# Optimization experiments

Hardware: AMD Instinct MI355X
Metric: run time of the kernel (lower is better)

The kernel has to match this reference:

```python
import jax, jax.numpy as jnp
import numpy as np

B, TY, ENC, EMB, DEC, V = 16, 255, 512, 256, 512, 32000
EPS = 1e-5


def _lstm(x, Wih, Whh, bih, bhh):
    # x: [B, T, Din]; torch gate order i, f, g, o; h0 = c0 = 0
    Bb = x.shape[0]
    H = Whh.shape[1]
    xw = jnp.einsum('btd,gd->btg', x, Wih) + bih + bhh  # [B, T, 4H]

    def step(carry, xt):
        h, c = carry
        g = xt + h @ Whh.T
        i, f, gg, o = jnp.split(g, 4, axis=-1)
        i = jax.nn.sigmoid(i)
        f = jax.nn.sigmoid(f)
        gg = jnp.tanh(gg)
        o = jax.nn.sigmoid(o)
        c = f * c + i * gg
        h = o * jnp.tanh(c)
        return (h, c), h

    h0 = jnp.zeros((Bb, H), x.dtype)
    _, hs = jax.lax.scan(step, (h0, h0), jnp.swapaxes(xw, 0, 1))
    return jnp.swapaxes(hs, 0, 1)  # [B, T, H]


def setup_inputs():
    key = jax.random.key(0)
    ks = jax.random.split(key, 16)
    s = 0.05
    rn = lambda k, sh: jax.random.normal(k, sh, jnp.float32)
    return {
        'x': rn(ks[0], (B, ENC)),
        'y': jax.random.randint(ks[1], (B, TY), 0, V),
        'fc1_w': rn(ks[2], (EMB, ENC)) * s,
        'fc1_b': rn(ks[3], (EMB,)) * s,
        'bn_g': jnp.ones((EMB,), jnp.float32),
        'bn_b': jnp.zeros((EMB,), jnp.float32),
        'emb': rn(ks[4], (V, EMB)) * s,
        'l1_Wih': rn(ks[5], (4 * DEC, EMB)) * s,
        'l1_Whh': rn(ks[6], (4 * DEC, DEC)) * s,
        'l1_bih': rn(ks[7], (4 * DEC,)) * s,
        'l1_bhh': rn(ks[8], (4 * DEC,)) * s,
        'attn_Wout': rn(ks[9], (DEC, 2 * DEC)) * s,
        'dc_Wih': rn(ks[10], (4 * DEC, DEC)) * s,
        'dc_Whh': rn(ks[11], (4 * DEC, DEC)) * s,
        'dc_bih': rn(ks[12], (4 * DEC,)) * s,
        'dc_bhh': rn(ks[13], (4 * DEC,)) * s,
        'fc2_w': rn(ks[14], (V, DEC)) * s,
        'fc2_b': rn(ks[15], (V,)) * s,
        'lengths': TY + 1,  # all sequences full length
    }


def reference(x, y, fc1_w, fc1_b, bn_g, bn_b, emb, l1_Wih, l1_Whh, l1_bih, l1_bhh,
              attn_Wout, dc_Wih, dc_Whh, dc_bih, dc_bhh, fc2_w, fc2_b, lengths):
    # fc1 + BatchNorm1d (training-mode batch stats, biased var)
    feat = x @ fc1_w.T + fc1_b                         # [B, EMB]
    mu = feat.mean(axis=0)
    var = feat.var(axis=0)
    feat = (feat - mu) / jnp.sqrt(var + EPS) * bn_g + bn_b
    # prepend feature to embedded tokens -> [B, L, EMB], L = TY + 1
    seq = jnp.concatenate([feat[:, None, :], emb[y]], axis=1)
    # first LSTM
    h = _lstm(seq, l1_Wih, l1_Whh, l1_bih, l1_bhh)     # [B, L, DEC]
    L = seq.shape[1]
    # causal dot-product self-attention (vectorized form of the python loop)
    scores = jnp.einsum('bqd,bkd->bqk', h, h)
    mask = jnp.tril(jnp.ones((L, L), bool))
    w = jax.nn.softmax(jnp.where(mask, scores, -1e30), axis=-1)
    mix = jnp.einsum('bqk,bkd->bqd', w, h)
    attn = jnp.tanh(jnp.concatenate([mix, h], axis=-1) @ attn_Wout.T)
    # decoder LSTM cell over attended features
    out = _lstm(attn, dc_Wih, dc_Whh, dc_bih, dc_bhh)  # [B, L, DEC]
    return out @ fc2_w.T + fc2_b                       # [B, L, V]
```

## Files before the change

kernel.cpp:

```cpp
#include <hip/hip_runtime.h>

#define BB 16
#define TY 255
#define ENC 512
#define EMBD 256
#define DEC 512
#define VV 32000
#define LL 256
#define M4 4096
#define GG 2048
#define SENT 0x7FC0

typedef unsigned short u16;
typedef __attribute__((ext_vector_type(8))) short short8;
typedef __attribute__((ext_vector_type(4))) float f32x4;
typedef __attribute__((ext_vector_type(4))) unsigned short u16x4;

__device__ __forceinline__ u16 f2bf(float f) {
  unsigned u = __float_as_uint(f);
  u += 0x7fff + ((u >> 16) & 1);
  return (u16)(u >> 16);
}
__device__ __forceinline__ f32x4 mfma16(short8 a, short8 b, f32x4 c) {
  return __builtin_amdgcn_mfma_f32_16x16x32_bf16(a, b, c, 0, 0, 0);
}
__device__ __forceinline__ float sigmoidf_(float x) { return 1.f / (1.f + expf(-x)); }

__device__ __forceinline__ void st_b32_dev(int* a, int v) {
  asm volatile("global_store_dword %0, %1, off sc1" :: "v"(a), "v"(v) : "memory");
}
__device__ __forceinline__ void gload_lds16(const u16* g, u16* l) {
  __builtin_amdgcn_global_load_lds(
      (const __attribute__((address_space(1))) void*)g,
      (__attribute__((address_space(3))) void*)l, 16, 0, 0);
}

template<bool BT, bool OBF, bool DOTANH, bool BIAS>
__global__ __launch_bounds__(256) void gemm_kernel(
    const u16* __restrict__ A, const u16* __restrict__ Bm, void* __restrict__ Cv,
    const float* __restrict__ bias,
    int K, int lda, int ldb, int ldc,
    long a_bs, long b_bs, long c_bs)
{
  __shared__ u16 As[64][72];
  __shared__ u16 Bs[64][72];
  const int tid = threadIdx.x;
  const long m0 = (long)blockIdx.y * 64, n0 = (long)blockIdx.x * 64;
  const int z = blockIdx.z;
  const u16* Ab = A + (long)z * a_bs;
  const u16* Bb = Bm + (long)z * b_bs;
  const int lane = tid & 63, w = tid >> 6;
  const int wm = w >> 1, wn = w & 1;
  f32x4 acc[2][2] = {};
  for (int k0 = 0; k0 < K; k0 += 64) {
#pragma unroll
    for (int i = 0; i < 2; i++) {
      int c = tid + 256 * i;
      int r = c >> 3, kk = (c & 7) << 3;
      *(short8*)&As[r][kk] = *(const short8*)&Ab[(m0 + r) * (long)lda + k0 + kk];
    }
    if (BT) {
#pragma unroll
      for (int i = 0; i < 2; i++) {
        int c = tid + 256 * i;
        int r = c >> 3, kk = (c & 7) << 3;
        *(short8*)&Bs[r][kk] = *(const short8*)&Bb[(n0 + r) * (long)ldb + k0 + kk];
      }
    } else {
#pragma unroll
      for (int i = 0; i < 2; i++) {
        int c = tid + 256 * i;
        int kk = c >> 3, nn = (c & 7) << 3;
        const u16* s = &Bb[(long)(k0 + kk) * ldb + n0 + nn];
#pragma unroll
        for (int j = 0; j < 8; j++) Bs[nn + j][kk] = s[j];
      }
    }
    __syncthreads();
#pragma unroll
    for (int kf = 0; kf < 2; kf++) {
      const int ko = kf * 32 + (lane >> 4) * 8;
      short8 a0 = *(const short8*)&As[wm * 32 + (lane & 15)][ko];
      short8 a1 = *(const short8*)&As[wm * 32 + 16 + (lane & 15)][ko];
      short8 b0 = *(const short8*)&Bs[wn * 32 + (lane & 15)][ko];
      short8 b1 = *(const short8*)&Bs[wn * 32 + 16 + (lane & 15)][ko];
      acc[0][0] = mfma16(a0, b0, acc[0][0]);
      acc[0][1] = mfma16(a0, b1, acc[0][1]);
      acc[1][0] = mfma16(a1, b0, acc[1][0]);
      acc[1][1] = mfma16(a1, b1, acc[1][1]);
    }
    __syncthreads();
  }
#pragma unroll
  for (int m = 0; m < 2; m++)
#pragma unroll
    for (int n = 0; n < 2; n++) {
#pragma unroll
      for (int r = 0; r < 4; r++) {
        long row = m0 + wm * 32 + m * 16 + (lane >> 4) * 4 + r;
        long col = n0 + wn * 32 + n * 16 + (lane & 15);
        float v = acc[m][n][r];
        if (BIAS) v += bias[col];
        if (DOTANH) v = tanhf(v);
        if (OBF) ((u16*)Cv)[(long)z * c_bs + row * ldc + col] = f2bf(v);
        else ((float*)Cv)[(long)z * c_bs + row * ldc + col] = v;
      }
    }
}

template<bool OBF, bool DOTANH, bool BIAS, bool CAUSAL3>
__global__ __launch_bounds__(256) void gemm128_kernel(
    const u16* __restrict__ A, const u16* __restrict__ Bm, void* __restrict__ Cv,
    const float* __restrict__ bias,
    int K, int lda, int ldb, int ldc,
    long a_bs, long b_bs, long c_bs)
{
  __shared__ u16 As[128 * 64];
  __shared__ u16 Bs[128 * 64];
  const int tid = threadIdx.x;
  long m0, n0;
  if (CAUSAL3) {
    int id = blockIdx.x;
    m0 = (id > 0) ? 128 : 0;
    n0 = (id > 1) ? 128 : 0;
  } else {
    m0 = (long)blockIdx.y * 128;
    n0 = (long)blockIdx.x * 128;
  }
  const int z = blockIdx.z;
  const u16* Ab = A + (long)z * a_bs;
  const u16* Bb = Bm + (long)z * b_bs;
  const int lane = tid & 63, w = tid >> 6;
  const int wm = w >> 1, wn = w & 1;
  const int rr = tid >> 3, kk = (tid & 7) << 3;
  f32x4 acc[4][4] = {};
  for (int k0 = 0; k0 < K; k0 += 64) {
#pragma unroll
    for (int i = 0; i < 4; i++) {
      gload_lds16(&Ab[(m0 + i * 32 + rr) * (long)lda + k0 + kk],
                  As + (i * 256 + (w << 6)) * 8);
      gload_lds16(&Bb[(n0 + i * 32 + rr) * (long)ldb + k0 + kk],
                  Bs + (i * 256 + (w << 6)) * 8);
    }
    __syncthreads();
#pragma unroll
    for (int kf = 0; kf < 2; kf++) {
      const int ko = kf * 32 + (lane >> 4) * 8;
      short8 a[4], b[4];
#pragma unroll
      for (int mi = 0; mi < 4; mi++)
        a[mi] = *(const short8*)&As[(wm * 64 + mi * 16 + (lane & 15)) * 64 + ko];
#pragma unroll
      for (int ni = 0; ni < 4; ni++)
        b[ni] = *(const short8*)&Bs[(wn * 64 + ni * 16 + (lane & 15)) * 64 + ko];
#pragma unroll
      for (int mi = 0; mi < 4; mi++)
#pragma unroll
        for (int ni = 0; ni < 4; ni++)
          acc[mi][ni] = mfma16(a[mi], b[ni], acc[mi][ni]);
    }
    __syncthreads();
  }
#pragma unroll
  for (int mi = 0; mi < 4; mi++)
#pragma unroll
    for (int ni = 0; ni < 4; ni++) {
#pragma unroll
      for (int r = 0; r < 4; r++) {
        long row = m0 + wm * 64 + mi * 16 + (lane >> 4) * 4 + r;
        long col = n0 + wn * 64 + ni * 16 + (lane & 15);
        float v = acc[mi][ni][r];
        if (BIAS) v += bias[col];
        if (DOTANH) v = tanhf(v);
        if (OBF) ((u16*)Cv)[(long)z * c_bs + row * ldc + col] = f2bf(v);
        else ((float*)Cv)[(long)z * c_bs + row * ldc + col] = v;
      }
    }
}

__global__ void sentinel_kernel(u16* __restrict__ p) {
  long i = ((long)blockIdx.x * 256 + threadIdx.x) * 8;
  short v = (i < 8192) ? (short)0 : (short)SENT;
  short8 s = {v, v, v, v, v, v, v, v};
  *(short8*)&p[i] = s;
}

template<int MODE>
__global__ __launch_bounds__(256) void lstm_kernel(
    const float* __restrict__ xw,
    const u16* __restrict__ Whh,
    u16* __restrict__ Hseq,
    u16* __restrict__ hout)
{
  const int nb = blockIdx.x;
  const int tid = threadIdx.x;
  const int lane = tid & 63, w = tid >> 6;
  __shared__ u16 hs[16][520];
  __shared__ float gbuf[16][64];
  const int ncol0 = nb * 64 + w * 16;
  short8 bfrag[16];
  {
    const u16* wr = Whh + (long)(ncol0 + (lane & 15)) * 512 + ((lane >> 4) * 8);
#pragma unroll
    for (int kf = 0; kf < 16; kf++) bfrag[kf] = *(const short8*)&wr[kf * 32];
  }
  const int b = tid >> 4, jl = tid & 15;
  const int jglob = nb * 16 + jl;
  int cc[4];
#pragma unroll
  for (int i = 0; i < 4; i++) cc[i] = (tid + i * 256 + nb * 32) & 1023;
  float c = 0.f;
  float4 xg = *(const float4*)&xw[((long)b * LL) * GG + nb * 64 + jl * 4];
  for (int t = 0; t < LL; t++) {
    const u16* Hin = Hseq + (long)t * 8192;
    short8 sv[4];
    int bad;
    do {
#pragma unroll
      for (int i = 0; i < 4; i++)
        asm volatile("global_load_dwordx4 %0, %1, off sc1"
                     : "=v"(sv[i]) : "v"(Hin + (cc[i] >> 6) * 512 + (cc[i] & 63) * 8));
      asm volatile("s_waitcnt vmcnt(0)" ::: "memory");
      __builtin_amdgcn_sched_barrier(0);
      bad = 0;
#pragma unroll
      for (int i = 0; i < 4; i++) {
        const int* dv = (const int*)&sv[i];
#pragma unroll
        for (int d = 0; d < 4; d++) bad |= ((dv[d] & 0xFFFF) == SENT);
      }
    } while (__any(bad != 0));
    __builtin_amdgcn_sched_barrier(0);
#pragma unroll
    for (int i = 0; i < 4; i++)
      *(short8*)&hs[cc[i] >> 6][(cc[i] & 63) * 8] = sv[i];
    __syncthreads();
    f32x4 acc0 = {}, acc1 = {};
#pragma unroll
    for (int kf = 0; kf < 8; kf++) {
      short8 a0 = *(const short8*)&hs[lane & 15][(lane >> 4) * 8 + (2 * kf) * 32];
      short8 a1 = *(const short8*)&hs[lane & 15][(lane >> 4) * 8 + (2 * kf + 1) * 32];
      acc0 = mfma16(a0, bfrag[2 * kf], acc0);
      acc1 = mfma16(a1, bfrag[2 * kf + 1], acc1);
    }
    f32x4 acc = acc0 + acc1;
#pragma unroll
    for (int r = 0; r < 4; r++)
      gbuf[(lane >> 4) * 4 + r][w * 16 + (lane & 15)] = acc[r];
    __syncthreads();
    float gi = sigmoidf_(gbuf[b][jl * 4 + 0] + xg.x);
    float gf = sigmoidf_(gbuf[b][jl * 4 + 1] + xg.y);
    float gg = tanhf(gbuf[b][jl * 4 + 2] + xg.z);
    float go = sigmoidf_(gbuf[b][jl * 4 + 3] + xg.w);
    c = gf * c + gi * gg;
    float h = go * tanhf(c);
    u16 hb = f2bf(h);
    unsigned hi16 = (unsigned)__shfl_down((int)(unsigned)hb, 1);
    if ((jl & 1) == 0) {
      int pk = (int)((unsigned)hb | (hi16 << 16));
      st_b32_dev((int*)&Hseq[((long)t + 1) * 8192 + b * 512 + jglob], pk);
    }
    if (MODE == 0) hout[((long)b * LL + t) * 1024 + 512 + jglob] = hb;
    else           hout[((long)b * LL + t) * 512 + jglob] = hb;
    if (t + 1 < LL)
      xg = *(const float4*)&xw[((long)b * LL + (t + 1)) * GG + nb * 64 + jl * 4];
  }
}

__global__ __launch_bounds__(256) void prep_kernel(
    const float* __restrict__ l1_Wih, const float* __restrict__ l1_Whh,
    const float* __restrict__ dc_Wih, const float* __restrict__ dc_Whh,
    const float* __restrict__ l1_bih, const float* __restrict__ l1_bhh,
    const float* __restrict__ dc_bih, const float* __restrict__ dc_bhh,
    const float* __restrict__ Wout,  const float* __restrict__ fc2_w,
    const int*   __restrict__ y,     const float* __restrict__ emb,
    const float* __restrict__ x,     const float* __restrict__ fc1_w,
    const float* __restrict__ fc1_b,
    u16* wih1, u16* whh1, u16* wih2, u16* whh2,
    float* b1p, float* b2p, u16* woutb, u16* fc2wb,
    u16* seqb, u16* Hseq, float* feat)
{
  const int bid = blockIdx.x;
  const int tid = threadIdx.x;
  if (bid < 8192) {
    int grp = bid >> 11, n = bid & 2047;
    const float* s; u16* d; int ldk;
    if (grp == 0)      { s = l1_Wih; d = wih1; ldk = EMBD; }
    else if (grp == 1) { s = l1_Whh; d = whh1; ldk = DEC; }
    else if (grp == 2) { s = dc_Wih; d = wih2; ldk = DEC; }
    else               { s = dc_Whh; d = whh2; ldk = DEC; }
    int r = (n & 3) * DEC + (n >> 2);
    for (int k = tid; k < ldk; k += 256)
      d[(long)n * ldk + k] = f2bf(s[(long)r * ldk + k]);
  } else if (bid < 8208) {
    int idx = bid - 8192;
    int n = (idx & 7) * 256 + tid;
    int r = (n & 3) * DEC + (n >> 2);
    if (idx < 8) b1p[n] = l1_bih[r] + l1_bhh[r];
    else         b2p[n] = dc_bih[r] + dc_bhh[r];
  } else if (bid < 8720) {
    long i = ((long)(bid - 8208) * 256 + tid) * 4;
    float4 v = *(const float4*)&Wout[i];
    u16x4 o = {f2bf(v.x), f2bf(v.y), f2bf(v.z), f2bf(v.w)};
    *(u16x4*)&woutb[i] = o;
  } else if (bid < 24720) {
    long i = ((long)(bid - 8720) * 256 + tid) * 4;
    float4 v = *(const float4*)&fc2_w[i];
    u16x4 o = {f2bf(v.x), f2bf(v.y), f2bf(v.z), f2bf(v.w)};
    *(u16x4*)&fc2wb[i] = o;
  } else if (bid < 28800) {
    int idx = bid - 24720;
    int t = idx % TY, bb = idx / TY;
    int tok = y[bb * TY + t];
    seqb[((long)bb * LL + 1 + t) * EMBD + tid] = f2bf(emb[(long)tok * EMBD + tid]);
  } else if (bid < 29828) {
    long i = ((long)(bid - 28800) * 256 + tid) * 8;
    short v = (i < 8192) ? (short)0 : (short)SENT;
    short8 s = {v, v, v, v, v, v, v, v};
    *(short8*)&Hseq[i] = s;
  } else {
    __shared__ float xs[ENC];
    int bb = bid - 29828;
    for (int k = tid; k < ENC; k += 256) xs[k] = x[bb * ENC + k];
    __syncthreads();
    float s = fc1_b[tid];
    const float* wr = fc1_w + (long)tid * ENC;
    for (int k = 0; k < ENC; k += 4) {
      float4 wv = *(const float4*)&wr[k];
      s += xs[k] * wv.x + xs[k + 1] * wv.y + xs[k + 2] * wv.z + xs[k + 3] * wv.w;
    }
    feat[bb * EMBD + tid] = s;
  }
}

__global__ void bn_embed0_kernel(const float* __restrict__ feat, const float* __restrict__ g,
                                 const float* __restrict__ bb, u16* __restrict__ seq) {
  int j = threadIdx.x;
  float mu = 0.f, m2 = 0.f;
  for (int i = 0; i < BB; i++) { float v = feat[i * EMBD + j]; mu += v; m2 += v * v; }
  mu *= (1.f / BB);
  float var = m2 * (1.f / BB) - mu * mu;
  float sc = g[j] * rsqrtf(var + 1e-5f);
  float sh = bb[j];
  for (int i = 0; i < BB; i++) {
    float v = (feat[i * EMBD + j] - mu) * sc + sh;
    seq[((long)i * LL) * EMBD + j] = f2bf(v);
  }
}

__global__ __launch_bounds__(256) void softmax_kernel(const float* __restrict__ sc,
                                                      u16* __restrict__ wsm) {
  int row = blockIdx.x;
  int q = row & (LL - 1);
  int k = threadIdx.x;
  __shared__ float red[8];
  float v = (k <= q) ? sc[(long)row * LL + k] : -3.4e38f;
  float m = v;
#pragma unroll
  for (int o = 32; o > 0; o >>= 1) m = fmaxf(m, __shfl_xor(m, o));
  if ((k & 63) == 0) red[k >> 6] = m;
  __syncthreads();
  m = fmaxf(fmaxf(red[0], red[1]), fmaxf(red[2], red[3]));
  float e = (k <= q) ? expf(v - m) : 0.f;
  float s = e;
#pragma unroll
  for (int o = 32; o > 0; o >>= 1) s += __shfl_xor(s, o);
  if ((k & 63) == 0) red[4 + (k >> 6)] = s;
  __syncthreads();
  s = red[4] + red[5] + red[6] + red[7];
  wsm[(long)row * LL + k] = f2bf(e / s);
}

extern "C" void kernel_launch(void* const* d_in, const int* in_sizes, int n_in,
                              void* d_out, int out_size, void* d_ws, size_t ws_size,
                              hipStream_t stream) {
  const float* x      = (const float*)d_in[0];
  const int*   y      = (const int*)d_in[1];
  const float* fc1_w  = (const float*)d_in[2];
  const float* fc1_b  = (const float*)d_in[3];
  const float* bn_g   = (const float*)d_in[4];
  const float* bn_b   = (const float*)d_in[5];
  const float* emb    = (const float*)d_in[6];
  const float* l1_Wih = (const float*)d_in[7];
  const float* l1_Whh = (const float*)d_in[8];
  const float* l1_bih = (const float*)d_in[9];
  const float* l1_bhh = (const float*)d_in[10];
  const float* Wout   = (const float*)d_in[11];
  const float* dc_Wih = (const float*)d_in[12];
  const float* dc_Whh = (const float*)d_in[13];
  const float* dc_bih = (const float*)d_in[14];
  const float* dc_bhh = (const float*)d_in[15];
  const float* fc2_w  = (const float*)d_in[16];
  const float* fc2_b  = (const float*)d_in[17];
  float* out = (float*)d_out;

  char* ws = (char*)d_ws;
  float* xw     = (float*)(ws + 0);
  u16*   seqb   = (u16*)(ws + 33554432);
  u16*   cat    = (u16*)(ws + 35651584);
  float* scores = (float*)(ws + 44040192);
  u16*   Hseq   = (u16*)(ws + 44040192);
  u16*   wsm    = (u16*)(ws + 48234496);
  u16*   attnb  = (u16*)(ws + 50331648);
  u16*   h2b    = (u16*)(ws + 54525952);
  u16*   wih1   = (u16*)(ws + 58720256);
  u16*   whh1   = (u16*)(ws + 59768832);
  u16*   wih2   = (u16*)(ws + 61865984);
  u16*   whh2   = (u16*)(ws + 63963136);
  u16*   woutb  = (u16*)(ws + 66060288);
  u16*   fc2wb  = (u16*)(ws + 67108864);
  float* b1p    = (float*)(ws + 99876864);
  float* b2p    = (float*)(ws + 99885056);
  float* feat   = (float*)(ws + 99893248);

  prep_kernel<<<29844, 256, 0, stream>>>(
      l1_Wih, l1_Whh, dc_Wih, dc_Whh, l1_bih, l1_bhh, dc_bih, dc_bhh,
      Wout, fc2_w, y, emb, x, fc1_w, fc1_b,
      wih1, whh1, wih2, whh2, b1p, b2p, woutb, fc2wb, seqb, Hseq, feat);
  bn_embed0_kernel<<<1, 256, 0, stream>>>(feat, bn_g, bn_b, seqb);

  gemm128_kernel<false, false, true, false><<<dim3(GG / 128, M4 / 128, 1), 256, 0, stream>>>(
      seqb, wih1, xw, b1p, EMBD, EMBD, EMBD, GG, 0, 0, 0);
  lstm_kernel<0><<<32, 256, 0, stream>>>(xw, whh1, Hseq, cat);
  gemm128_kernel<false, false, false, true><<<dim3(3, 1, BB), 256, 0, stream>>>(
      cat + 512, cat + 512, scores, nullptr, DEC, 1024, 1024, LL,
      (long)LL * 1024, (long)LL * 1024, (long)LL * LL);
  softmax_kernel<<<M4, 256, 0, stream>>>(scores, wsm);
  gemm_kernel<false, true, false, false><<<dim3(DEC / 64, LL / 64, BB), 256, 0, stream>>>(
      wsm, cat + 512, cat, nullptr, LL, LL, 1024, 1024,
      (long)LL * LL, (long)LL * 1024, (long)LL * 1024);
  gemm128_kernel<true, true, false, false><<<dim3(DEC / 128, M4 / 128, 1), 256, 0, stream>>>(
      cat, woutb, attnb, nullptr, 1024, 1024, 1024, DEC, 0, 0, 0);
  gemm128_kernel<false, false, true, false><<<dim3(GG / 128, M4 / 128, 1), 256, 0, stream>>>(
      attnb, wih2, xw, b2p, DEC, DEC, DEC, GG, 0, 0, 0);
  sentinel_kernel<<<1028, 256, 0, stream>>>(Hseq);
  lstm_kernel<1><<<32, 256, 0, stream>>>(xw, whh2, Hseq, h2b);
  gemm128_kernel<false, false, true, false><<<dim3(VV / 128, M4 / 128, 1), 256, 0, stream>>>(
      h2b, fc2wb, out, fc2_b, DEC, DEC, DEC, VV, 0, 0, 0);
}
```

Before: 1.445 ms.

## Co-locate LSTM recurrence blocks on a single XCD for local-cache handoff

```diff
diff --git a/kernel.cpp b/kernel.cpp
--- a/kernel.cpp
+++ b/kernel.cpp
@@ -26,9 +26,6 @@
 }
 __device__ __forceinline__ float sigmoidf_(float x) { return 1.f / (1.f + expf(-x)); }
 
-__device__ __forceinline__ void st_b32_dev(int* a, int v) {
-  asm volatile("global_store_dword %0, %1, off sc1" :: "v"(a), "v"(v) : "memory");
-}
 __device__ __forceinline__ void gload_lds16(const u16* g, u16* l) {
   __builtin_amdgcn_global_load_lds(
       (const __attribute__((address_space(1))) void*)g,
@@ -190,10 +187,39 @@
     const float* __restrict__ xw,
     const u16* __restrict__ Whh,
     u16* __restrict__ Hseq,
-    u16* __restrict__ hout)
+    u16* __restrict__ hout,
+    int* __restrict__ sync)
 {
-  const int nb = blockIdx.x;
+  __shared__ int s_nb;
   const int tid = threadIdx.x;
+  if (tid == 0) {
+    int xcc;
+    asm volatile("s_getreg_b32 %0, hwreg(20, 0, 32)" : "=s"(xcc));
+    xcc &= 7;
+    int slot = __hip_atomic_fetch_add(&sync[xcc * 8], 1,
+                                      __ATOMIC_RELAXED, __HIP_MEMORY_SCOPE_AGENT);
+    if (slot == 31) {
+      int e0 = 0;
+      __hip_atomic_compare_exchange_strong(&sync[64], &e0, xcc + 1,
+          __ATOMIC_RELAXED, __ATOMIC_RELAXED, __HIP_MEMORY_SCOPE_AGENT);
+    }
+    int win, spins = 0;
+    while ((win = __hip_atomic_load(&sync[64], __ATOMIC_RELAXED,
+                                    __HIP_MEMORY_SCOPE_AGENT)) == 0) {
+      __builtin_amdgcn_s_sleep(2);
+      if (++spins == 100000) {
+        int e0 = 0;
+        __hip_atomic_compare_exchange_strong(&sync[64], &e0, -1,
+            __ATOMIC_RELAXED, __ATOMIC_RELAXED, __HIP_MEMORY_SCOPE_AGENT);
+      }
+    }
+    s_nb = (win == -1) ? (((int)blockIdx.x < 32) ? (int)blockIdx.x : -1)
+                       : ((win == xcc + 1 && slot < 32) ? slot : -1);
+  }
+  __syncthreads();
+  const int nb = s_nb;
+  if (nb < 0) return;
+
   const int lane = tid & 63, w = tid >> 6;
   __shared__ u16 hs[16][520];
   __shared__ float gbuf[16][64];
@@ -214,8 +240,22 @@
   for (int t = 0; t < LL; t++) {
     const u16* Hin = Hseq + (long)t * 8192;
     short8 sv[4];
-    int bad;
-    do {
+    for (;;) {
+      int bad;
+#pragma unroll
+      for (int i = 0; i < 4; i++)
+        asm volatile("global_load_dwordx4 %0, %1, off sc0"
+                     : "=v"(sv[i]) : "v"(Hin + (cc[i] >> 6) * 512 + (cc[i] & 63) * 8));
+      asm volatile("s_waitcnt vmcnt(0)" ::: "memory");
+      __builtin_amdgcn_sched_barrier(0);
+      bad = 0;
+#pragma unroll
+      for (int i = 0; i < 4; i++) {
+        const int* dv = (const int*)&sv[i];
+#pragma unroll
+        for (int d = 0; d < 4; d++) bad |= ((dv[d] & 0xFFFF) == SENT);
+      }
+      if (!__any(bad != 0)) break;
 #pragma unroll
       for (int i = 0; i < 4; i++)
         asm volatile("global_load_dwordx4 %0, %1, off sc1"
@@ -229,7 +269,8 @@
 #pragma unroll
         for (int d = 0; d < 4; d++) bad |= ((dv[d] & 0xFFFF) == SENT);
       }
-    } while (__any(bad != 0));
+      if (!__any(bad != 0)) break;
+    }
     __builtin_amdgcn_sched_barrier(0);
 #pragma unroll
     for (int i = 0; i < 4; i++)
@@ -258,7 +299,9 @@
     unsigned hi16 = (unsigned)__shfl_down((int)(unsigned)hb, 1);
     if ((jl & 1) == 0) {
       int pk = (int)((unsigned)hb | (hi16 << 16));
-      st_b32_dev((int*)&Hseq[((long)t + 1) * 8192 + b * 512 + jglob], pk);
+      int* pa = (int*)&Hseq[((long)t + 1) * 8192 + b * 512 + jglob];
+      asm volatile("global_store_dword %0, %1, off sc0" :: "v"(pa), "v"(pk) : "memory");
+      asm volatile("global_store_dword %0, %1, off sc1" :: "v"(pa), "v"(pk) : "memory");
     }
     if (MODE == 0) hout[((long)b * LL + t) * 1024 + 512 + jglob] = hb;
     else           hout[((long)b * LL + t) * 512 + jglob] = hb;
@@ -412,6 +455,10 @@
   float* b1p    = (float*)(ws + 99876864);
   float* b2p    = (float*)(ws + 99885056);
   float* feat   = (float*)(ws + 99893248);
+  int*   sync1  = (int*)(ws + 99909632);
+  int*   sync2  = (int*)(ws + 99910144);
+
+  hipMemsetAsync(ws + 99909632, 0, 1024, stream);
 
   prep_kernel<<<29844, 256, 0, stream>>>(
       l1_Wih, l1_Whh, dc_Wih, dc_Whh, l1_bih, l1_bhh, dc_bih, dc_bhh,
@@ -421,7 +468,7 @@
 
   gemm128_kernel<false, false, true, false><<<dim3(GG / 128, M4 / 128, 1), 256, 0, stream>>>(
       seqb, wih1, xw, b1p, EMBD, EMBD, EMBD, GG, 0, 0, 0);
-  lstm_kernel<0><<<32, 256, 0, stream>>>(xw, whh1, Hseq, cat);
+  lstm_kernel<0><<<256, 256, 0, stream>>>(xw, whh1, Hseq, cat, sync1);
   gemm128_kernel<false, false, false, true><<<dim3(3, 1, BB), 256, 0, stream>>>(
       cat + 512, cat + 512, scores, nullptr, DEC, 1024, 1024, LL,
       (long)LL * 1024, (long)LL * 1024, (long)LL * LL);
@@ -434,7 +481,7 @@
   gemm128_kernel<false, false, true, false><<<dim3(GG / 128, M4 / 128, 1), 256, 0, stream>>>(
       attnb, wih2, xw, b2p, DEC, DEC, DEC, GG, 0, 0, 0);
   sentinel_kernel<<<1028, 256, 0, stream>>>(Hseq);
-  lstm_kernel<1><<<32, 256, 0, stream>>>(xw, whh2, Hseq, h2b);
+  lstm_kernel<1><<<256, 256, 0, stream>>>(xw, whh2, Hseq, h2b, sync2);
   gemm128_kernel<false, false, true, false><<<dim3(VV / 128, M4 / 128, 1), 256, 0, stream>>>(
       h2b, fc2wb, out, fc2_b, DEC, DEC, DEC, VV, 0, 0, 0);
 }
```

Measured after the change: 1.934 ms. 1.34x slower.
